# Optimization experiments

Hardware: AMD Instinct MI355X
Metric: run time of the kernel (lower is better)

Reference implementation:

```python
import jax, jax.numpy as jnp
import numpy as np

B, T, D = 8, 1024, 768
N_HEAD = 12
HEAD_DIM = D // N_HEAD


def setup_inputs() -> dict:
    key = jax.random.key(0)
    k1, k2, k3, k4, k5 = jax.random.split(key, 5)
    x = jax.random.normal(k1, (B, T, D), dtype=jnp.float32)
    # c_attn: Linear(D, 3D); c_proj: Linear(D, D). Stored as (in, out) for x @ W.
    s_attn = 1.0 / np.sqrt(D)
    W_attn = jax.random.uniform(k2, (D, 3 * D), dtype=jnp.float32, minval=-s_attn, maxval=s_attn)
    b_attn = jax.random.uniform(k3, (3 * D,), dtype=jnp.float32, minval=-s_attn, maxval=s_attn)
    W_proj = jax.random.uniform(k4, (D, D), dtype=jnp.float32, minval=-s_attn, maxval=s_attn)
    b_proj = jax.random.uniform(k5, (D,), dtype=jnp.float32, minval=-s_attn, maxval=s_attn)
    return {"x": x, "W_attn": W_attn, "b_attn": b_attn, "W_proj": W_proj, "b_proj": b_proj}


def reference(x, W_attn, b_attn, W_proj, b_proj):
    Bs, Ts, Ds = x.shape
    qkv = x @ W_attn + b_attn  # [B, T, 3D]
    Q, K, V = jnp.split(qkv, 3, axis=2)
    # [B, H, T, hd]
    Q = Q.reshape(Bs, Ts, N_HEAD, HEAD_DIM).transpose(0, 2, 1, 3)
    K = K.reshape(Bs, Ts, N_HEAD, HEAD_DIM).transpose(0, 2, 1, 3)
    V = V.reshape(Bs, Ts, N_HEAD, HEAD_DIM).transpose(0, 2, 1, 3)
    scale = HEAD_DIM ** (-0.5)
    scores = jnp.einsum('bhqd,bhkd->bhqk', Q, K) * scale  # [B, H, T, T]
    causal = jnp.tril(jnp.ones((Ts, Ts), dtype=bool))
    scores = jnp.where(causal[None, None, :, :], scores, -jnp.inf)
    probs = jax.nn.softmax(scores, axis=-1)
    attn = jnp.einsum('bhqk,bhkd->bhqd', probs, V)  # [B, H, T, hd]
    attn = attn.transpose(0, 2, 1, 3).reshape(Bs, Ts, Ds)
    return attn @ W_proj + b_proj
```

## Files before the change

### kernel.cpp

```cpp
#include <hip/hip_runtime.h>
#include <hip/hip_bf16.h>

#define B_ 8
#define T_ 1024
#define D_ 768
#define NH 12
#define HD 64

typedef __bf16 bf16x8 __attribute__((ext_vector_type(8)));
typedef __bf16 bf16x4 __attribute__((ext_vector_type(4)));
typedef float f32x4 __attribute__((ext_vector_type(4)));
typedef short s16x4 __attribute__((ext_vector_type(4)));

__device__ __forceinline__ float fast_exp2(float x) {
  return __builtin_amdgcn_exp2f(x);
}

__device__ __forceinline__ f32x4 mfma32(bf16x8 a, bf16x8 b, f32x4 c) {
  return __builtin_amdgcn_mfma_f32_16x16x32_bf16(a, b, c, 0, 0, 0);
}

__device__ __forceinline__ f32x4 mfma16(bf16x4 a, bf16x4 b, f32x4 c) {
  union U { bf16x4 h; s16x4 s; };
  U ua; ua.h = a;
  U ub; ub.h = b;
  return __builtin_amdgcn_mfma_f32_16x16x16bf16_1k(ua.s, ub.s, c, 0, 0, 0);
}

__device__ __forceinline__ void gload_lds16(const void* g, void* l) {
  __builtin_amdgcn_global_load_lds((const __attribute__((address_space(1))) unsigned int*)g,
                                   (__attribute__((address_space(3))) unsigned int*)l, 16, 0, 0);
}

__global__ void xconv_kernel(const float* __restrict__ x, __bf16* __restrict__ xb, int n8) {
  int i = blockIdx.x * 256 + threadIdx.x;
  if (i >= n8) return;
  const float4* xf = (const float4*)x;
  float4 a = xf[i * 2], b = xf[i * 2 + 1];
  bf16x8 v;
  v[0] = (__bf16)a.x; v[1] = (__bf16)a.y; v[2] = (__bf16)a.z; v[3] = (__bf16)a.w;
  v[4] = (__bf16)b.x; v[5] = (__bf16)b.y; v[6] = (__bf16)b.z; v[7] = (__bf16)b.w;
  *(bf16x8*)&xb[(size_t)i * 8] = v;
}

__global__ void wtrans_kernel(const float* __restrict__ W, __bf16* __restrict__ WT, int K, int N) {
  __shared__ float tile[32][33];
  int t = threadIdx.x, col = t & 31, r0 = t >> 5;
  int n0 = blockIdx.x * 32, k0 = blockIdx.y * 32;
#pragma unroll
  for (int p = 0; p < 4; p++) {
    int r = r0 + p * 8;
    tile[r][col] = W[(size_t)(k0 + r) * N + n0 + col];
  }
  __syncthreads();
#pragma unroll
  for (int p = 0; p < 4; p++) {
    int r = r0 + p * 8;
    WT[(size_t)(n0 + r) * K + k0 + col] = (__bf16)tile[col][r];
  }
}

template <int EPI>
__global__ __launch_bounds__(256) void gemm_kernel(const __bf16* __restrict__ A,
                                                   const __bf16* __restrict__ BT,
                                                   const float* __restrict__ bias,
                                                   void* __restrict__ Cout,
                                                   int M, int N, int K) {
  __shared__ __align__(16) __bf16 Asm[128][72];
  __shared__ __align__(16) __bf16 Bsm[128][72];
  int tid = threadIdx.x;
  int wave = tid >> 6, lane = tid & 63, g = lane >> 4, l15 = lane & 15;
  int wr = wave >> 1, wc = wave & 1;
  int m0 = blockIdx.y * 128, n0 = blockIdx.x * 128;
  int srow = tid >> 3, sk8 = tid & 7;
  const __bf16* Ag = A + (size_t)(m0 + srow) * K + sk8 * 8;
  const __bf16* Bg = BT + (size_t)(n0 + srow) * K + sk8 * 8;

  f32x4 zz = {0.0f, 0.0f, 0.0f, 0.0f};
  f32x4 acc[4][4];
#pragma unroll
  for (int m = 0; m < 4; m++)
#pragma unroll
    for (int n = 0; n < 4; n++) acc[m][n] = zz;

  int nk = K >> 6;
  bf16x8 Av[4], Bv[4];
#pragma unroll
  for (int p = 0; p < 4; p++) {
    Av[p] = *(const bf16x8*)(Ag + (size_t)p * 32 * K);
    Bv[p] = *(const bf16x8*)(Bg + (size_t)p * 32 * K);
  }
  for (int kt = 0; kt < nk; kt++) {
    __syncthreads();
#pragma unroll
    for (int p = 0; p < 4; p++) {
      *(bf16x8*)&Asm[srow + p * 32][sk8 * 8] = Av[p];
      *(bf16x8*)&Bsm[srow + p * 32][sk8 * 8] = Bv[p];
    }
    __syncthreads();
    if (kt + 1 < nk) {
#pragma unroll
      for (int p = 0; p < 4; p++) {
        Av[p] = *(const bf16x8*)(Ag + (kt + 1) * 64 + (size_t)p * 32 * K);
        Bv[p] = *(const bf16x8*)(Bg + (kt + 1) * 64 + (size_t)p * 32 * K);
      }
    }
#pragma unroll
    for (int ks = 0; ks < 2; ks++) {
      bf16x8 af[4], bfr[4];
#pragma unroll
      for (int m = 0; m < 4; m++) af[m] = *(const bf16x8*)&Asm[wr * 64 + m * 16 + l15][ks * 32 + g * 8];
#pragma unroll
      for (int n = 0; n < 4; n++) bfr[n] = *(const bf16x8*)&Bsm[wc * 64 + n * 16 + l15][ks * 32 + g * 8];
#pragma unroll
      for (int m = 0; m < 4; m++)
#pragma unroll
        for (int n = 0; n < 4; n++)
          acc[m][n] = __builtin_amdgcn_mfma_f32_16x16x32_bf16(af[m], bfr[n], acc[m][n], 0, 0, 0);
    }
  }
#pragma unroll
  for (int n = 0; n < 4; n++) {
    int gcol = n0 + wc * 64 + n * 16 + l15;
    float bv = bias[gcol];
#pragma unroll
    for (int m = 0; m < 4; m++) {
      int grow0 = m0 + wr * 64 + m * 16 + g * 4;
#pragma unroll
      for (int r = 0; r < 4; r++) {
        float v = acc[m][n][r] + bv;
        if (EPI == 0)
          ((__bf16*)Cout)[(size_t)(grow0 + r) * N + gcol] = (__bf16)v;
        else
          ((float*)Cout)[(size_t)(grow0 + r) * N + gcol] = v;
      }
    }
  }
}

__global__ void vtrepack_kernel(const __bf16* __restrict__ qkv, __bf16* __restrict__ VT) {
  __shared__ __align__(16) __bf16 tl[64][72];
  int bh = blockIdx.y;
  int b = bh / NH, h = bh % NH;
  int t0 = blockIdx.x * 64;
  int tid = threadIdx.x;
  int tr = tid >> 3, d8 = tid & 7;
#pragma unroll
  for (int p = 0; p < 2; p++) {
    int trow = tr + p * 32;
    bf16x8 v = *(const bf16x8*)&qkv[(size_t)(b * T_ + t0 + trow) * (3 * D_) + 2 * D_ + h * HD + d8 * 8];
#pragma unroll
    for (int e = 0; e < 8; e++) tl[d8 * 8 + e][trow] = v[e];
  }
  __syncthreads();
  int t8 = tid & 7;
#pragma unroll
  for (int p = 0; p < 2; p++) {
    int d = (tid >> 3) + p * 32;
    *(bf16x8*)&VT[((size_t)bh * HD + d) * T_ + t0 + t8 * 8] = *(const bf16x8*)&tl[d][t8 * 8];
  }
}

#define SCL 0.1803368801111204f

__global__ __launch_bounds__(256, 4) void attn_kernel(const __bf16* __restrict__ qkv,
                                                      const __bf16* __restrict__ VT,
                                                      __bf16* __restrict__ attn_out) {
  __shared__ __align__(16) __bf16 sm[2][2][4096];
  int tid = threadIdx.x;
  int wave = tid >> 6, lane = tid & 63, g = lane >> 4, l15 = lane & 15;
  int bh = blockIdx.x;
  int b = bh / NH, h = bh % NH;
  int qb = 15 - blockIdx.y;
  int q0w = qb * 64 + wave * 16;
  int nkt = qb + 1;
  int s0 = (bh + qb) % nkt;

  int kr = tid >> 3, cc = (tid & 7) ^ ((tid >> 3) & 7);
  const __bf16* Kst = qkv + (size_t)(b * T_ + kr) * (3 * D_) + D_ + h * HD + cc * 8;
  const __bf16* Vst = VT + ((size_t)bh * HD + kr) * T_ + cc * 8;
  __bf16* ldsK0 = &sm[0][0][wave * 512];
  __bf16* ldsV0 = &sm[0][1][wave * 512];
  __bf16* ldsK1 = &sm[1][0][wave * 512];
  __bf16* ldsV1 = &sm[1][1][wave * 512];

  auto stage = [&](int t, int bf) {
    size_t ko = (size_t)(t * 64) * (3 * D_);
    int vo = t * 64;
    __bf16* lk = bf ? ldsK1 : ldsK0;
    __bf16* lv = bf ? ldsV1 : ldsV0;
    gload_lds16(Kst + ko, lk);
    gload_lds16(Kst + ko + (size_t)32 * (3 * D_), lk + 2048);
    gload_lds16(Vst + vo, lv);
    gload_lds16(Vst + vo + 32 * T_, lv + 2048);
  };

  const __bf16* Qp = qkv + (size_t)(b * T_ + q0w + l15) * (3 * D_) + h * HD;
  bf16x8 qlo = *(const bf16x8*)(Qp + g * 8);
  bf16x8 qhi = *(const bf16x8*)(Qp + 32 + g * 8);

  f32x4 zz = {0.0f, 0.0f, 0.0f, 0.0f};
  f32x4 o0 = zz, o1 = zz, o2 = zz, o3 = zz;
  float m = -1e30f, l = 0.0f;
  int sw = l15 & 7;
  int clo = (g ^ sw) * 8;
  int chi = ((4 + g) ^ sw) * 8;

  stage(s0, 0);
  __syncthreads();

  int cur = 0;
  for (int i = 0; i < nkt; i++) {
    int kt = s0 + i;
    if (kt >= nkt) kt -= nkt;
    if (i + 1 < nkt) stage(kt + 1 == nkt ? 0 : kt + 1, cur ^ 1);

    const __bf16* Kb = &sm[cur][0][0];
    f32x4 s[4];
#pragma unroll
    for (int kg = 0; kg < 4; kg++) {
      int rb = (kg * 16 + l15) * 64;
      bf16x8 kf = *(const bf16x8*)(Kb + rb + clo);
      bf16x8 kh = *(const bf16x8*)(Kb + rb + chi);
      s[kg] = mfma32(kf, qlo, zz);
      s[kg] = mfma32(kh, qhi, s[kg]);
    }

    float v[16];
#pragma unroll
    for (int kg = 0; kg < 4; kg++)
#pragma unroll
      for (int r = 0; r < 4; r++) v[kg * 4 + r] = s[kg][r] * SCL;
    if (kt == qb) {
      int thr = wave * 16 + l15;
#pragma unroll
      for (int kg = 0; kg < 4; kg++)
#pragma unroll
        for (int r = 0; r < 4; r++)
          if (kg * 16 + g * 4 + r > thr) v[kg * 4 + r] = -1e30f;
    }
    float m0a = fmaxf(fmaxf(v[0], v[1]), fmaxf(v[2], v[3]));
    float m1a = fmaxf(fmaxf(v[4], v[5]), fmaxf(v[6], v[7]));
    float m2a = fmaxf(fmaxf(v[8], v[9]), fmaxf(v[10], v[11]));
    float m3a = fmaxf(fmaxf(v[12], v[13]), fmaxf(v[14], v[15]));
    float mx = fmaxf(fmaxf(m0a, m1a), fmaxf(m2a, m3a));
    mx = fmaxf(mx, __shfl_xor(mx, 16));
    mx = fmaxf(mx, __shfl_xor(mx, 32));
    float mnew = fmaxf(m, mx);
    float corr = fast_exp2(m - mnew);
    float p[16], sum = 0.0f;
#pragma unroll
    for (int i2 = 0; i2 < 16; i2++) { p[i2] = fast_exp2(v[i2] - mnew); sum += p[i2]; }
    sum += __shfl_xor(sum, 16);
    sum += __shfl_xor(sum, 32);
    l = l * corr + sum;
    m = mnew;
    o0 *= corr; o1 *= corr; o2 *= corr; o3 *= corr;
    bf16x4 pk[4];
#pragma unroll
    for (int kg = 0; kg < 4; kg++) {
      pk[kg][0] = (__bf16)p[kg * 4 + 0];
      pk[kg][1] = (__bf16)p[kg * 4 + 1];
      pk[kg][2] = (__bf16)p[kg * 4 + 2];
      pk[kg][3] = (__bf16)p[kg * 4 + 3];
    }

    const __bf16* Vb = &sm[cur][1][0];
    int vhalf = (g & 1) * 4;
    int vc = g >> 1;
#pragma unroll
    for (int dq = 0; dq < 4; dq++) {
      int drow = (dq * 16 + l15) * 64;
#pragma unroll
      for (int ks = 0; ks < 4; ks++) {
        bf16x4 vf = *(const bf16x4*)(Vb + drow + ((ks * 2 + vc) ^ sw) * 8 + vhalf);
        f32x4* op = (dq == 0) ? &o0 : (dq == 1) ? &o1 : (dq == 2) ? &o2 : &o3;
        *op = mfma16(vf, pk[ks], *op);
      }
    }

    __syncthreads();
    cur ^= 1;
  }

  float invl = 1.0f / l;
  __bf16* outp = attn_out + (size_t)(b * T_ + q0w + l15) * D_ + h * HD + g * 4;
  bf16x4 t0 = {(__bf16)(o0[0] * invl), (__bf16)(o0[1] * invl), (__bf16)(o0[2] * invl), (__bf16)(o0[3] * invl)};
  bf16x4 t1 = {(__bf16)(o1[0] * invl), (__bf16)(o1[1] * invl), (__bf16)(o1[2] * invl), (__bf16)(o1[3] * invl)};
  bf16x4 t2 = {(__bf16)(o2[0] * invl), (__bf16)(o2[1] * invl), (__bf16)(o2[2] * invl), (__bf16)(o2[3] * invl)};
  bf16x4 t3 = {(__bf16)(o3[0] * invl), (__bf16)(o3[1] * invl), (__bf16)(o3[2] * invl), (__bf16)(o3[3] * invl)};
  *(bf16x4*)(outp) = t0;
  *(bf16x4*)(outp + 16) = t1;
  *(bf16x4*)(outp + 32) = t2;
  *(bf16x4*)(outp + 48) = t3;
}

extern "C" void kernel_launch(void* const* d_in, const int* in_sizes, int n_in,
                              void* d_out, int out_size, void* d_ws, size_t ws_size,
                              hipStream_t stream) {
  (void)in_sizes; (void)n_in; (void)out_size; (void)ws_size;
  const float* x = (const float*)d_in[0];
  const float* W_attn = (const float*)d_in[1];
  const float* b_attn = (const float*)d_in[2];
  const float* W_proj = (const float*)d_in[3];
  const float* b_proj = (const float*)d_in[4];

  char* ws = (char*)d_ws;
  __bf16* xb  = (__bf16*)(ws + 0);
  __bf16* WaT = (__bf16*)(ws + 12582912);
  __bf16* WpT = (__bf16*)(ws + 16121856);
  __bf16* qkv = (__bf16*)(ws + 17301504);
  __bf16* VTb = (__bf16*)(ws + 55050240);
  __bf16* att = (__bf16*)(ws + 67633152);

  xconv_kernel<<<dim3(3072), 256, 0, stream>>>(x, xb, 786432);
  wtrans_kernel<<<dim3(72, 24), 256, 0, stream>>>(W_attn, WaT, 768, 2304);
  wtrans_kernel<<<dim3(24, 24), 256, 0, stream>>>(W_proj, WpT, 768, 768);
  gemm_kernel<0><<<dim3(18, 64), 256, 0, stream>>>(xb, WaT, b_attn, qkv, 8192, 2304, 768);
  vtrepack_kernel<<<dim3(16, 96), 256, 0, stream>>>(qkv, VTb);
  attn_kernel<<<dim3(96, 16), 256, 0, stream>>>(qkv, VTb, att);
  gemm_kernel<1><<<dim3(6, 64), 256, 0, stream>>>(att, WpT, b_proj, d_out, 8192, 768, 768);
}
```

Before: 120.5 us.

## Use direct global-to-LDS loads with XOR swizzle and XCD-aware block remap in GEMM

The GEMM kernel now loads A and B tiles directly from global memory into LDS through a gload_lds16 helper, replacing the register-staged prefetch. The LDS layout becomes unpadded with an XOR swizzle to avoid bank conflicts. Block indices are flattened and remapped so consecutive tiles land on the same XCD, aiming for better L2 reuse. The register prefetch of the next tile is dropped, so global loads are no longer overlapped with compute across iterations. The code also depends on gload_lds16 being defined in the unseen part of the file.

```diff
diff --git a/kernel.cpp b/kernel.cpp
--- a/kernel.cpp
+++ b/kernel.cpp
@@ -65,16 +65,25 @@
                                                    const __bf16* __restrict__ BT,
                                                    const float* __restrict__ bias,
                                                    void* __restrict__ Cout,
-                                                   int M, int N, int K) {
-  __shared__ __align__(16) __bf16 Asm[128][72];
-  __shared__ __align__(16) __bf16 Bsm[128][72];
+                                                   int M, int N, int K, int nbx) {
+  __shared__ __align__(16) __bf16 Asm[128 * 64];
+  __shared__ __align__(16) __bf16 Bsm[128 * 64];
   int tid = threadIdx.x;
   int wave = tid >> 6, lane = tid & 63, g = lane >> 4, l15 = lane & 15;
   int wr = wave >> 1, wc = wave & 1;
-  int m0 = blockIdx.y * 128, n0 = blockIdx.x * 128;
-  int srow = tid >> 3, sk8 = tid & 7;
-  const __bf16* Ag = A + (size_t)(m0 + srow) * K + sk8 * 8;
-  const __bf16* Bg = BT + (size_t)(n0 + srow) * K + sk8 * 8;
+
+  int wg = blockIdx.x;
+  int cpx = gridDim.x >> 3;
+  int wg2 = (wg & 7) * cpx + (wg >> 3);
+  int bx = wg2 % nbx, by = wg2 / nbx;
+  int m0 = by * 128, n0 = bx * 128;
+
+  int srow = tid >> 3;
+  int cc = (tid & 7) ^ ((tid >> 3) & 7);
+  const __bf16* Ag = A + (size_t)(m0 + srow) * K + cc * 8;
+  const __bf16* Bg = BT + (size_t)(n0 + srow) * K + cc * 8;
+  __bf16* ldsA = Asm + wave * 512;
+  __bf16* ldsB = Bsm + wave * 512;
 
   f32x4 zz = {0.0f, 0.0f, 0.0f, 0.0f};
   f32x4 acc[4][4];
@@ -84,40 +93,34 @@
     for (int n = 0; n < 4; n++) acc[m][n] = zz;
 
   int nk = K >> 6;
-  bf16x8 Av[4], Bv[4];
-#pragma unroll
-  for (int p = 0; p < 4; p++) {
-    Av[p] = *(const bf16x8*)(Ag + (size_t)p * 32 * K);
-    Bv[p] = *(const bf16x8*)(Bg + (size_t)p * 32 * K);
-  }
+  int swr = l15 & 7;
   for (int kt = 0; kt < nk; kt++) {
+#pragma unroll
+    for (int i = 0; i < 4; i++) {
+      gload_lds16(Ag + (size_t)(i * 32) * K + kt * 64, ldsA + i * 2048);
+      gload_lds16(Bg + (size_t)(i * 32) * K + kt * 64, ldsB + i * 2048);
+    }
     __syncthreads();
-#pragma unroll
-    for (int p = 0; p < 4; p++) {
-      *(bf16x8*)&Asm[srow + p * 32][sk8 * 8] = Av[p];
-      *(bf16x8*)&Bsm[srow + p * 32][sk8 * 8] = Bv[p];
-    }
-    __syncthreads();
-    if (kt + 1 < nk) {
-#pragma unroll
-      for (int p = 0; p < 4; p++) {
-        Av[p] = *(const bf16x8*)(Ag + (kt + 1) * 64 + (size_t)p * 32 * K);
-        Bv[p] = *(const bf16x8*)(Bg + (kt + 1) * 64 + (size_t)p * 32 * K);
-      }
-    }
 #pragma unroll
     for (int ks = 0; ks < 2; ks++) {
       bf16x8 af[4], bfr[4];
 #pragma unroll
-      for (int m = 0; m < 4; m++) af[m] = *(const bf16x8*)&Asm[wr * 64 + m * 16 + l15][ks * 32 + g * 8];
-#pragma unroll
-      for (int n = 0; n < 4; n++) bfr[n] = *(const bf16x8*)&Bsm[wc * 64 + n * 16 + l15][ks * 32 + g * 8];
+      for (int m = 0; m < 4; m++) {
+        int row = wr * 64 + m * 16 + l15;
+        af[m] = *(const bf16x8*)&Asm[row * 64 + ((ks * 4 + g) ^ swr) * 8];
+      }
+#pragma unroll
+      for (int n = 0; n < 4; n++) {
+        int row = wc * 64 + n * 16 + l15;
+        bfr[n] = *(const bf16x8*)&Bsm[row * 64 + ((ks * 4 + g) ^ swr) * 8];
+      }
 #pragma unroll
       for (int m = 0; m < 4; m++)
 #pragma unroll
         for (int n = 0; n < 4; n++)
           acc[m][n] = __builtin_amdgcn_mfma_f32_16x16x32_bf16(af[m], bfr[n], acc[m][n], 0, 0, 0);
     }
+    __syncthreads();
   }
 #pragma unroll
   for (int n = 0; n < 4; n++) {
@@ -316,8 +319,8 @@
   xconv_kernel<<<dim3(3072), 256, 0, stream>>>(x, xb, 786432);
   wtrans_kernel<<<dim3(72, 24), 256, 0, stream>>>(W_attn, WaT, 768, 2304);
   wtrans_kernel<<<dim3(24, 24), 256, 0, stream>>>(W_proj, WpT, 768, 768);
-  gemm_kernel<0><<<dim3(18, 64), 256, 0, stream>>>(xb, WaT, b_attn, qkv, 8192, 2304, 768);
+  gemm_kernel<0><<<dim3(1152), 256, 0, stream>>>(xb, WaT, b_attn, qkv, 8192, 2304, 768, 18);
   vtrepack_kernel<<<dim3(16, 96), 256, 0, stream>>>(qkv, VTb);
   attn_kernel<<<dim3(96, 16), 256, 0, stream>>>(qkv, VTb, att);
-  gemm_kernel<1><<<dim3(6, 64), 256, 0, stream>>>(att, WpT, b_proj, d_out, 8192, 768, 768);
-}
+  gemm_kernel<1><<<dim3(384), 256, 0, stream>>>(att, WpT, b_proj, d_out, 8192, 768, 768, 6);
+}
```

Measured after the change: 125.8 us. 1.04x slower.
